# Kernel optimization log

Measured on AMD Instinct MI355X. Metric: run time of the kernel, lower is better.

## Reference

```python
import jax, jax.numpy as jnp
import numpy as np

KNOW = 128
EXER_N = 20000
STU_N = 50000
N_EDGES = 1000000
N_EDGES_P = 950000
BATCH = 8192
SOFT_PARA = 0.2
EPS = 1e-8


def setup_inputs() -> dict:
    key = jax.random.key(0)
    ks = jax.random.split(key, 10)
    return {
        'stu_emb': jax.random.normal(ks[0], (STU_N, KNOW), jnp.float32) * 0.1,
        'exer_emb': jax.random.normal(ks[1], (EXER_N, KNOW), jnp.float32) * 0.1,
        'W_ue': jax.random.normal(ks[2], (KNOW, KNOW), jnp.float32) / np.sqrt(KNOW),
        'W_ue_per': jax.random.normal(ks[3], (KNOW, KNOW), jnp.float32) / np.sqrt(KNOW),
        'W_deep': jax.random.normal(ks[4], (KNOW, KNOW), jnp.float32) / np.sqrt(KNOW),
        'src_e': jax.random.randint(ks[5], (N_EDGES,), 0, EXER_N),
        'dst_e': jax.random.randint(ks[6], (N_EDGES,), 0, STU_N),
        'src_p': jax.random.randint(ks[7], (N_EDGES_P,), 0, EXER_N),
        'dst_p': jax.random.randint(ks[8], (N_EDGES_P,), 0, STU_N),
        'stu_id': jax.random.randint(ks[9], (BATCH,), 0, STU_N),
    }


def _graph_layer(exer, W, src, dst):
    # u_from_e: messages flow exercise -> student. Linear transform then mean-aggregate.
    msg = exer[src] @ W                                   # [E_edges, K]
    agg = jax.ops.segment_sum(msg, dst, num_segments=STU_N)
    deg = jax.ops.segment_sum(jnp.ones_like(dst, jnp.float32), dst, num_segments=STU_N)
    return agg / jnp.maximum(deg, 1.0)[:, None]           # [STU_N, K]


def reference(stu_emb, exer_emb, W_ue, W_ue_per, W_deep, src_e, dst_e, src_p, dst_p, stu_id):
    # ExpressionDooubleEva: two parallel graph views
    stu1 = stu_emb + _graph_layer(exer_emb, W_ue, src_e, dst_e)
    stu_per = stu_emb + _graph_layer(exer_emb, W_ue_per, src_p, dst_p)
    # ExpressionSingleEva (u_from_e output is overwritten by u_from_e_deep in source)
    stu2 = stu1 + _graph_layer(exer_emb, W_deep, src_e, dst_e)
    stu2_per = stu_per + _graph_layer(exer_emb, W_deep, src_e, dst_e)

    b1 = stu2[stu_id]          # [B, K]
    b2 = stu2_per[stu_id]      # [B, K]
    n1 = b1 / jnp.linalg.norm(b1, axis=1, keepdims=True)
    n2 = b2 / jnp.linalg.norm(b2, axis=1, keepdims=True)
    sim = (n1 @ n2.T) / SOFT_PARA                         # [B, B]
    # faithful to source: numerator = exp(diag(sim)), denominator = sum of RAW sim row
    diag_exp = jnp.exp(jnp.diagonal(sim))
    row_sum = jnp.sum(sim, axis=1)
    ratio = diag_exp / (row_sum + EPS)
    ssl_loss = jnp.mean(-jnp.log(jnp.maximum(ratio, EPS)))
    return stu2, ssl_loss
```

## Files before the change

### kernel.cpp

```cpp
#include <hip/hip_runtime.h>
#include <math.h>

#define KNOW 128
#define STU_N 50000
#define EXER_N 20000
#define BATCH 8192
#define NE 1000000
#define NEP 950000
#define SOFT_INV 5.0f
#define EPS 1e-8f

#define CAP 64
#define NBIN 256
#define SPB 196
#define SSE 4608
#define SSP 1536
#define P1B 256
#define P1T 1024
#define WPB 24

typedef unsigned short u16;
typedef unsigned int u32;

typedef __attribute__((ext_vector_type(8))) short bf16x8;
typedef __attribute__((ext_vector_type(4))) float f32x4;

__device__ __forceinline__ u16 f2bf(float f) {
  union { float f; u32 u; } v;
  v.f = f;
  u32 r = (v.u + 0x7FFFu + ((v.u >> 16) & 1u)) >> 16;
  return (u16)r;
}
__device__ __forceinline__ float bflo(u32 u) {
  union { u32 u; float f; } v;
  v.u = u << 16;
  return v.f;
}
__device__ __forceinline__ float bfhi(u32 u) {
  union { u32 u; float f; } v;
  v.u = u & 0xFFFF0000u;
  return v.f;
}
__device__ __forceinline__ float bfu(u16 h) {
  union { u32 u; float f; } v;
  v.u = ((u32)h) << 16;
  return v.f;
}

__global__ void set_flags(const int* __restrict__ stu_id,
                          unsigned char* __restrict__ flag,
                          int* __restrict__ gcur_e, int* __restrict__ gcur_p) {
  int i = blockIdx.x * blockDim.x + threadIdx.x;
  if (i < BATCH) flag[stu_id[i]] = 1;
  if (i < NBIN) {
    gcur_e[i] = i * SSE;
    gcur_p[i] = i * SSP;
  }
}

__global__ __launch_bounds__(256) void prep_split(
    const float* __restrict__ exer, const float* __restrict__ W_ue,
    const float* __restrict__ W_per, const float* __restrict__ W_deep,
    u16* __restrict__ Ah, u16* __restrict__ Al, u16* __restrict__ WTh,
    u16* __restrict__ WTl) {
  int b = blockIdx.x;
  if (b < WPB) {
    int plane = b >> 3;
    int slab = b & 7;
    int t = threadIdx.x;
    int n = t & 127;
    int k0 = slab * 16 + (t >> 7) * 8;
    const float* W0 = (plane == 0) ? W_ue : (plane == 1) ? W_per : W_deep;
    float x[8];
#pragma unroll
    for (int j = 0; j < 8; ++j) {
      float v = W0[(k0 + j) * KNOW + n];
      if (plane == 0) v += W_deep[(k0 + j) * KNOW + n];
      x[j] = v;
    }
    u16 hi[8], lo[8];
#pragma unroll
    for (int j = 0; j < 8; ++j) {
      u16 h = f2bf(x[j]);
      hi[j] = h;
      lo[j] = f2bf(x[j] - bfu(h));
    }
    size_t base = ((size_t)plane * KNOW + n) * KNOW + k0;
    uint4 H = {(u32)hi[0] | ((u32)hi[1] << 16), (u32)hi[2] | ((u32)hi[3] << 16),
               (u32)hi[4] | ((u32)hi[5] << 16), (u32)hi[6] | ((u32)hi[7] << 16)};
    uint4 L = {(u32)lo[0] | ((u32)lo[1] << 16), (u32)lo[2] | ((u32)lo[3] << 16),
               (u32)lo[4] | ((u32)lo[5] << 16), (u32)lo[6] | ((u32)lo[7] << 16)};
    *(uint4*)(WTh + base) = H;
    *(uint4*)(WTl + base) = L;
  } else {
    size_t i = ((size_t)(b - WPB) * 256 + threadIdx.x) * 4;
    float4 v = *(const float4*)(exer + i);
    u16 h0 = f2bf(v.x), h1 = f2bf(v.y), h2 = f2bf(v.z), h3 = f2bf(v.w);
    ushort4 H = {h0, h1, h2, h3};
    ushort4 L = {f2bf(v.x - bfu(h0)), f2bf(v.y - bfu(h1)), f2bf(v.z - bfu(h2)),
                 f2bf(v.w - bfu(h3))};
    *(ushort4*)(Ah + i) = H;
    *(ushort4*)(Al + i) = L;
  }
}

#define BM_T 80

__global__ __launch_bounds__(512) void transform_mfma(
    const u16* __restrict__ Ah, const u16* __restrict__ Al,
    const u16* __restrict__ WTh, const u16* __restrict__ WTl,
    u16* __restrict__ X_sum, u16* __restrict__ X_per,
    u16* __restrict__ X_deep) {
  int t = threadIdx.x;
  int wv = t >> 6;
  int l = t & 63;
  int bn = l & 15;
  int kb = l >> 4;
  int row0 = blockIdx.x * BM_T;
  int n = wv * 16 + bn;

#pragma unroll 1
  for (int which = 0; which < 3; ++which) {
    u16* outp = (which == 0) ? X_sum : (which == 1) ? X_per : X_deep;
    const u16* wth = WTh + (size_t)which * KNOW * KNOW;
    const u16* wtl = WTl + (size_t)which * KNOW * KNOW;
    bf16x8 bh[4], bl[4];
#pragma unroll
    for (int ks = 0; ks < 4; ++ks) {
      int off = n * KNOW + ks * 32 + kb * 8;
      bh[ks] = *(const bf16x8*)(wth + off);
      bl[ks] = *(const bf16x8*)(wtl + off);
    }
#pragma unroll 1
    for (int rt = 0; rt < 5; ++rt) {
      int row = row0 + rt * 16 + bn;
      const u16* ap = Ah + (size_t)row * KNOW + kb * 8;
      const u16* alp = Al + (size_t)row * KNOW + kb * 8;
      f32x4 acc = {0.f, 0.f, 0.f, 0.f};
#pragma unroll
      for (int ks = 0; ks < 4; ++ks) {
        bf16x8 af = *(const bf16x8*)(ap + ks * 32);
        bf16x8 lf = *(const bf16x8*)(alp + ks * 32);
        acc = __builtin_amdgcn_mfma_f32_16x16x32_bf16(af, bh[ks], acc, 0, 0, 0);
        acc = __builtin_amdgcn_mfma_f32_16x16x32_bf16(lf, bh[ks], acc, 0, 0, 0);
        acc = __builtin_amdgcn_mfma_f32_16x16x32_bf16(af, bl[ks], acc, 0, 0, 0);
      }
      int orow = row0 + rt * 16 + kb * 4;
#pragma unroll
      for (int r = 0; r < 4; ++r)
        outp[(size_t)(orow + r) * KNOW + n] = f2bf(acc[r]);
    }
  }
}

__global__ __launch_bounds__(P1T) void bin_pass1(
    const int* __restrict__ dst_e, const int* __restrict__ src_e,
    const int* __restrict__ dst_p, const int* __restrict__ src_p,
    const unsigned char* __restrict__ flag, int* __restrict__ gcur_e,
    int* __restrict__ gcur_p, u32* __restrict__ stag_e,
    u32* __restrict__ stag_p) {
  __shared__ int cntE[NBIN], cntP[NBIN];
  __shared__ int baseE[NBIN], baseP[NBIN];
  __shared__ int curE[NBIN], curP[NBIN];
  int t = threadIdx.x;
  if (t < NBIN) {
    cntE[t] = 0;
    cntP[t] = 0;
  }
  __syncthreads();
  int b = blockIdx.x;
  int e0 = (int)((long long)NE * b / P1B);
  int e1 = (int)((long long)NE * (b + 1) / P1B);
  int p0 = (int)((long long)NEP * b / P1B);
  int p1 = (int)((long long)NEP * (b + 1) / P1B);
  for (int i = e0 + t; i < e1; i += P1T) {
    int d = __builtin_nontemporal_load(&dst_e[i]);
    atomicAdd(&cntE[d / SPB], 1);
  }
  for (int i = p0 + t; i < p1; i += P1T) {
    int d = __builtin_nontemporal_load(&dst_p[i]);
    if (flag[d]) atomicAdd(&cntP[d / SPB], 1);
  }
  __syncthreads();
  if (t < NBIN) {
    baseE[t] = atomicAdd(&gcur_e[t], cntE[t]);
    baseP[t] = atomicAdd(&gcur_p[t], cntP[t]);
    curE[t] = 0;
    curP[t] = 0;
  }
  __syncthreads();
  for (int i = e0 + t; i < e1; i += P1T) {
    int d = __builtin_nontemporal_load(&dst_e[i]);
    int s = __builtin_nontemporal_load(&src_e[i]);
    int bin = d / SPB;
    int pos = baseE[bin] + atomicAdd(&curE[bin], 1);
    if (pos < (bin + 1) * SSE)
      stag_e[pos] = ((u32)(d - bin * SPB) << 16) | (u32)s;
  }
  for (int i = p0 + t; i < p1; i += P1T) {
    int d = __builtin_nontemporal_load(&dst_p[i]);
    if (!flag[d]) continue;
    int s = __builtin_nontemporal_load(&src_p[i]);
    int bin = d / SPB;
    int pos = baseP[bin] + atomicAdd(&curP[bin], 1);
    if (pos < (bin + 1) * SSP)
      stag_p[pos] = ((u32)(d - bin * SPB) << 16) | (u32)s;
  }
}

__global__ __launch_bounds__(256) void bin_pass2(
    const u32* __restrict__ stag_e, const u32* __restrict__ stag_p,
    const int* __restrict__ gcur_e, const int* __restrict__ gcur_p,
    u16* __restrict__ bucket_e, u16* __restrict__ bucket_p,
    int* __restrict__ cnt_e, int* __restrict__ cnt_p) {
  __shared__ u16 be[SPB * CAP];
  __shared__ u16 bp[SPB * CAP];
  __shared__ int ce[SPB], cp[SPB];
  int t = threadIdx.x;
  int bin = blockIdx.x;
  for (int i = t; i < SPB; i += 256) {
    ce[i] = 0;
    cp[i] = 0;
  }
  __syncthreads();
  int ne = gcur_e[bin] - bin * SSE;
  if (ne > SSE) ne = SSE;
  int np = gcur_p[bin] - bin * SSP;
  if (np > SSP) np = SSP;
  const u32* se = stag_e + (size_t)bin * SSE;
  for (int i = t; i < ne; i += 256) {
    u32 w = se[i];
    int dl = (int)(w >> 16), s = (int)(w & 0xFFFFu);
    int slot = atomicAdd(&ce[dl], 1);
    if (slot < CAP) be[dl * CAP + slot] = (u16)s;
  }
  const u32* sp = stag_p + (size_t)bin * SSP;
  for (int i = t; i < np; i += 256) {
    u32 w = sp[i];
    int dl = (int)(w >> 16), s = (int)(w & 0xFFFFu);
    int slot = atomicAdd(&cp[dl], 1);
    if (slot < CAP) bp[dl * CAP + slot] = (u16)s;
  }
  __syncthreads();
  int s0 = bin * SPB;
  int nstu = STU_N - s0;
  if (nstu > SPB) nstu = SPB;
  if (nstu <= 0) return;
  int nvec = nstu * CAP * 2 / 16;
  const uint4* bev = (const uint4*)be;
  uint4* ge = (uint4*)(bucket_e + (size_t)s0 * CAP);
  for (int i = t; i < nvec; i += 256) ge[i] = bev[i];
  const uint4* bpv = (const uint4*)bp;
  uint4* gp = (uint4*)(bucket_p + (size_t)s0 * CAP);
  for (int i = t; i < nvec; i += 256) gp[i] = bpv[i];
  for (int i = t; i < nstu; i += 256) {
    cnt_e[s0 + i] = ce[i];
    cnt_p[s0 + i] = cp[i];
  }
}

__global__ __launch_bounds__(256) void stu2_gather(
    const float* __restrict__ stu_emb, const u16* __restrict__ X_sum,
    const u16* __restrict__ bucket, const int* __restrict__ cnt,
    float* __restrict__ out) {
  int wv = threadIdx.x >> 6;
  int l = threadIdx.x & 63;
  int s = blockIdx.x * 4 + wv;
  if (s >= STU_N) return;
  int deg = cnt[s];
  int e = (deg < CAP) ? deg : CAP;
  const u16* brow = bucket + (size_t)s * CAP;
  u32 bval = brow[l];
  int g = l >> 4;
  int c = l & 15;
  float acc[8] = {};
  for (int i = g; i < e; i += 8) {
    int r1 = __shfl((int)bval, i);
    const uint4 q1 = *(const uint4*)(X_sum + (size_t)r1 * KNOW + c * 8);
    int i2 = i + 4;
    int j2 = (i2 < e) ? i2 : (e - 1);
    int r2 = __shfl((int)bval, j2);
    const uint4 q2 = *(const uint4*)(X_sum + (size_t)r2 * KNOW + c * 8);
    float w2 = (i2 < e) ? 1.0f : 0.0f;
    acc[0] += bflo(q1.x) + w2 * bflo(q2.x);
    acc[1] += bfhi(q1.x) + w2 * bfhi(q2.x);
    acc[2] += bflo(q1.y) + w2 * bflo(q2.y);
    acc[3] += bfhi(q1.y) + w2 * bfhi(q2.y);
    acc[4] += bflo(q1.z) + w2 * bflo(q2.z);
    acc[5] += bfhi(q1.z) + w2 * bfhi(q2.z);
    acc[6] += bflo(q1.w) + w2 * bflo(q2.w);
    acc[7] += bfhi(q1.w) + w2 * bfhi(q2.w);
  }
#pragma unroll
  for (int j = 0; j < 8; ++j) {
    float v = acc[j];
    v += __shfl_xor(v, 16);
    v += __shfl_xor(v, 32);
    acc[j] = v;
  }
  if (l < 16) {
    float inv = 1.0f / fmaxf((float)deg, 1.0f);
    float4 se0 = *(const float4*)(stu_emb + (size_t)s * KNOW + c * 8);
    float4 se1 = *(const float4*)(stu_emb + (size_t)s * KNOW + c * 8 + 4);
    float4 o0 = {se0.x + acc[0] * inv, se0.y + acc[1] * inv,
                 se0.z + acc[2] * inv, se0.w + acc[3] * inv};
    float4 o1 = {se1.x + acc[4] * inv, se1.y + acc[5] * inv,
                 se1.z + acc[6] * inv, se1.w + acc[7] * inv};
    *(float4*)(out + (size_t)s * KNOW + c * 8) = o0;
    *(float4*)(out + (size_t)s * KNOW + c * 8 + 4) = o1;
  }
}

__global__ __launch_bounds__(128) void batch_kernel(
    const float* __restrict__ stu_emb, const float* __restrict__ stu2,
    const u16* __restrict__ X_per, const u16* __restrict__ X_deep,
    const u16* __restrict__ bucket_p, const int* __restrict__ cnt_p,
    const u16* __restrict__ bucket_e, const int* __restrict__ cnt_e,
    const int* __restrict__ stu_id, float* __restrict__ n1,
    float* __restrict__ n2, float* __restrict__ diag) {
  __shared__ float red[128];
  int i = blockIdx.x;
  int k = threadIdx.x;
  int sid = stu_id[i];

  int degp = cnt_p[sid];
  int ep = (degp < CAP) ? degp : CAP;
  const u16* brp = bucket_p + (size_t)sid * CAP;
  float accp = 0.0f;
  int j = 0;
  for (; j + 4 <= ep; j += 4) {
    int s0 = brp[j], s1 = brp[j + 1], s2 = brp[j + 2], s3 = brp[j + 3];
    accp += bfu(X_per[(size_t)s0 * KNOW + k]);
    accp += bfu(X_per[(size_t)s1 * KNOW + k]);
    accp += bfu(X_per[(size_t)s2 * KNOW + k]);
    accp += bfu(X_per[(size_t)s3 * KNOW + k]);
  }
  for (; j < ep; ++j) accp += bfu(X_per[(size_t)brp[j] * KNOW + k]);
  accp /= fmaxf((float)degp, 1.0f);

  int degd = cnt_e[sid];
  int ed = (degd < CAP) ? degd : CAP;
  const u16* brd = bucket_e + (size_t)sid * CAP;
  float accd = 0.0f;
  j = 0;
  for (; j + 4 <= ed; j += 4) {
    int s0 = brd[j], s1 = brd[j + 1], s2 = brd[j + 2], s3 = brd[j + 3];
    accd += bfu(X_deep[(size_t)s0 * KNOW + k]);
    accd += bfu(X_deep[(size_t)s1 * KNOW + k]);
    accd += bfu(X_deep[(size_t)s2 * KNOW + k]);
    accd += bfu(X_deep[(size_t)s3 * KNOW + k]);
  }
  for (; j < ed; ++j) accd += bfu(X_deep[(size_t)brd[j] * KNOW + k]);
  accd /= fmaxf((float)degd, 1.0f);

  float b1 = stu2[(size_t)sid * KNOW + k];
  float b2 = stu_emb[(size_t)sid * KNOW + k] + accp + accd;

  red[k] = b1 * b1;
  __syncthreads();
  for (int s = 64; s > 0; s >>= 1) {
    if (k < s) red[k] += red[k + s];
    __syncthreads();
  }
  float norm1 = sqrtf(red[0]);
  __syncthreads();
  red[k] = b2 * b2;
  __syncthreads();
  for (int s = 64; s > 0; s >>= 1) {
    if (k < s) red[k] += red[k + s];
    __syncthreads();
  }
  float norm2 = sqrtf(red[0]);

  float v1 = b1 / norm1;
  float v2 = b2 / norm2;
  n1[(size_t)i * KNOW + k] = v1;
  n2[(size_t)i * KNOW + k] = v2;

  __syncthreads();
  red[k] = v1 * v2;
  __syncthreads();
  for (int s = 64; s > 0; s >>= 1) {
    if (k < s) red[k] += red[k + s];
    __syncthreads();
  }
  if (k == 0) diag[i] = red[0];
}

__global__ __launch_bounds__(128) void s2_reduce(const float* __restrict__ n2,
                                                 float* __restrict__ S2) {
  int k = threadIdx.x;
  int r0 = blockIdx.x * (BATCH / 64);
  float acc = 0.0f;
  for (int r = 0; r < BATCH / 64; ++r) acc += n2[(size_t)(r0 + r) * KNOW + k];
  atomicAdd(&S2[k], acc);
}

#define L2BLKS 64
__global__ __launch_bounds__(256) void loss2(const float* __restrict__ n1,
                                             const float* __restrict__ diag,
                                             const float* __restrict__ S2,
                                             float* __restrict__ loss) {
  __shared__ float s2s[KNOW];
  int t = threadIdx.x;
  if (t < KNOW) s2s[t] = S2[t];
  __syncthreads();
  int wave = t >> 6, lane = t & 63;
  const int rows_per_wave = BATCH / (L2BLKS * 4);
  int r0 = (blockIdx.x * 4 + wave) * rows_per_wave;
  float acc = 0.0f;
  for (int r = r0; r < r0 + rows_per_wave; ++r) {
    float v = n1[(size_t)r * KNOW + lane] * s2s[lane] +
              n1[(size_t)r * KNOW + 64 + lane] * s2s[64 + lane];
#pragma unroll
    for (int off = 32; off > 0; off >>= 1) v += __shfl_down(v, off);
    if (lane == 0) {
      float rs = v * SOFT_INV;
      float dg = diag[r] * SOFT_INV;
      float ratio = expf(dg) / (rs + EPS);
      acc += -logf(fmaxf(ratio, EPS));
    }
  }
  if (lane == 0) atomicAdd(loss, acc);
}

__global__ void finalize_kernel(const float* __restrict__ loss,
                                float* __restrict__ out) {
  out[(size_t)STU_N * KNOW] = loss[0] * (1.0f / (float)BATCH);
}

extern "C" void kernel_launch(void* const* d_in, const int* in_sizes, int n_in,
                              void* d_out, int out_size, void* d_ws,
                              size_t ws_size, hipStream_t stream) {
  const float* stu_emb = (const float*)d_in[0];
  const float* exer_emb = (const float*)d_in[1];
  const float* W_ue = (const float*)d_in[2];
  const float* W_ue_per = (const float*)d_in[3];
  const float* W_deep = (const float*)d_in[4];
  const int* src_e = (const int*)d_in[5];
  const int* dst_e = (const int*)d_in[6];
  const int* src_p = (const int*)d_in[7];
  const int* dst_p = (const int*)d_in[8];
  const int* stu_id = (const int*)d_in[9];
  float* out = (float*)d_out;

  char* wsb = (char*)d_ws;
  float* S2 = (float*)wsb;
  float* loss = S2 + KNOW;
  unsigned char* flag = (unsigned char*)(loss + 1);
  size_t zero_bytes = (size_t)(flag + ((STU_N + 3) & ~3) - (unsigned char*)wsb);
  int* cnt_e = (int*)(flag + ((STU_N + 3) & ~3));
  int* cnt_p = cnt_e + STU_N;
  int* gcur_e = cnt_p + STU_N;
  int* gcur_p = gcur_e + NBIN;
  u16* X_sum = (u16*)(gcur_p + NBIN);
  u16* X_per = X_sum + (size_t)EXER_N * KNOW;
  u16* X_deep = X_per + (size_t)EXER_N * KNOW;
  u16* bucket_e = X_deep + (size_t)EXER_N * KNOW;
  u16* bucket_p = bucket_e + (size_t)STU_N * CAP;
  u32* stag_e = (u32*)(bucket_p + (size_t)STU_N * CAP);
  u32* stag_p = stag_e + (size_t)NBIN * SSE;
  float* n1 = (float*)(stag_p + (size_t)NBIN * SSP);
  float* n2 = n1 + (size_t)BATCH * KNOW;
  float* diag = n2 + (size_t)BATCH * KNOW;

  u16* Ah = (u16*)stag_e;
  u16* Al = (u16*)n1;
  u16* WTh = Al + (size_t)EXER_N * KNOW;
  u16* WTl = WTh + (size_t)3 * KNOW * KNOW;

  hipMemsetAsync(d_ws, 0, zero_bytes, stream);

  set_flags<<<(BATCH + 255) / 256, 256, 0, stream>>>(stu_id, flag, gcur_e,
                                                     gcur_p);

  prep_split<<<WPB + EXER_N * KNOW / 1024, 256, 0, stream>>>(
      exer_emb, W_ue, W_ue_per, W_deep, Ah, Al, WTh, WTl);

  transform_mfma<<<EXER_N / BM_T, 512, 0, stream>>>(Ah, Al, WTh, WTl, X_sum,
                                                    X_per, X_deep);

  bin_pass1<<<P1B, P1T, 0, stream>>>(dst_e, src_e, dst_p, src_p, flag, gcur_e,
                                     gcur_p, stag_e, stag_p);

  bin_pass2<<<NBIN, 256, 0, stream>>>(stag_e, stag_p, gcur_e, gcur_p, bucket_e,
                                      bucket_p, cnt_e, cnt_p);

  stu2_gather<<<(STU_N + 3) / 4, 256, 0, stream>>>(stu_emb, X_sum, bucket_e,
                                                   cnt_e, out);

  batch_kernel<<<BATCH, 128, 0, stream>>>(stu_emb, out, X_per, X_deep,
                                          bucket_p, cnt_p, bucket_e, cnt_e,
                                          stu_id, n1, n2, diag);

  s2_reduce<<<64, 128, 0, stream>>>(n2, S2);

  loss2<<<L2BLKS, 256, 0, stream>>>(n1, diag, S2, loss);

  finalize_kernel<<<1, 1, 0, stream>>>(loss, out);
}
```

Before: 280.9 us.

## Replace two-pass binned bucketing with single-pass global-atomic bucket build

Removes the two-kernel binning scheme (per-block shared-memory histograms, staging buffer, then per-bin LDS bucket assembly) and builds the per-student CSR-like buckets in one kernel using global atomicAdd on per-student counters with direct scattered u16 writes. This drops a kernel launch and the staging round-trip but adds about 1M contended global atomics and uncoalesced 2-byte scattered stores. The gather loop also replaces the multiply-by-mask with a branch for the second row, and the workspace is re-laid out so the split buffers no longer alias the staging area.

```diff
diff --git a/kernel.cpp b/kernel.cpp
--- a/kernel.cpp
+++ b/kernel.cpp
@@ -11,12 +11,7 @@
 #define EPS 1e-8f
 
 #define CAP 64
-#define NBIN 256
-#define SPB 196
-#define SSE 4608
-#define SSP 1536
-#define P1B 256
-#define P1T 1024
+#define BBB 1024
 #define WPB 24
 
 typedef unsigned short u16;
@@ -48,13 +43,31 @@
 }
 
 __global__ void set_flags(const int* __restrict__ stu_id,
-                          unsigned char* __restrict__ flag,
-                          int* __restrict__ gcur_e, int* __restrict__ gcur_p) {
+                          unsigned char* __restrict__ flag) {
   int i = blockIdx.x * blockDim.x + threadIdx.x;
   if (i < BATCH) flag[stu_id[i]] = 1;
-  if (i < NBIN) {
-    gcur_e[i] = i * SSE;
-    gcur_p[i] = i * SSP;
+}
+
+__global__ __launch_bounds__(256) void build_buckets(
+    const int* __restrict__ dst_e, const int* __restrict__ src_e,
+    const int* __restrict__ dst_p, const int* __restrict__ src_p,
+    const unsigned char* __restrict__ flag, int* __restrict__ cnt_e,
+    int* __restrict__ cnt_p, u16* __restrict__ bucket_e,
+    u16* __restrict__ bucket_p) {
+  int tid = blockIdx.x * 256 + threadIdx.x;
+  const int stride = BBB * 256;
+  for (int i = tid; i < NE; i += stride) {
+    int d = __builtin_nontemporal_load(&dst_e[i]);
+    int s = __builtin_nontemporal_load(&src_e[i]);
+    int slot = atomicAdd(&cnt_e[d], 1);
+    if (slot < CAP) bucket_e[(size_t)d * CAP + slot] = (u16)s;
+  }
+  for (int i = tid; i < NEP; i += stride) {
+    int d = __builtin_nontemporal_load(&dst_p[i]);
+    if (!flag[d]) continue;
+    int s = __builtin_nontemporal_load(&src_p[i]);
+    int slot = atomicAdd(&cnt_p[d], 1);
+    if (slot < CAP) bucket_p[(size_t)d * CAP + slot] = (u16)s;
   }
 }
 
@@ -150,112 +163,6 @@
       for (int r = 0; r < 4; ++r)
         outp[(size_t)(orow + r) * KNOW + n] = f2bf(acc[r]);
     }
-  }
-}
-
-__global__ __launch_bounds__(P1T) void bin_pass1(
-    const int* __restrict__ dst_e, const int* __restrict__ src_e,
-    const int* __restrict__ dst_p, const int* __restrict__ src_p,
-    const unsigned char* __restrict__ flag, int* __restrict__ gcur_e,
-    int* __restrict__ gcur_p, u32* __restrict__ stag_e,
-    u32* __restrict__ stag_p) {
-  __shared__ int cntE[NBIN], cntP[NBIN];
-  __shared__ int baseE[NBIN], baseP[NBIN];
-  __shared__ int curE[NBIN], curP[NBIN];
-  int t = threadIdx.x;
-  if (t < NBIN) {
-    cntE[t] = 0;
-    cntP[t] = 0;
-  }
-  __syncthreads();
-  int b = blockIdx.x;
-  int e0 = (int)((long long)NE * b / P1B);
-  int e1 = (int)((long long)NE * (b + 1) / P1B);
-  int p0 = (int)((long long)NEP * b / P1B);
-  int p1 = (int)((long long)NEP * (b + 1) / P1B);
-  for (int i = e0 + t; i < e1; i += P1T) {
-    int d = __builtin_nontemporal_load(&dst_e[i]);
-    atomicAdd(&cntE[d / SPB], 1);
-  }
-  for (int i = p0 + t; i < p1; i += P1T) {
-    int d = __builtin_nontemporal_load(&dst_p[i]);
-    if (flag[d]) atomicAdd(&cntP[d / SPB], 1);
-  }
-  __syncthreads();
-  if (t < NBIN) {
-    baseE[t] = atomicAdd(&gcur_e[t], cntE[t]);
-    baseP[t] = atomicAdd(&gcur_p[t], cntP[t]);
-    curE[t] = 0;
-    curP[t] = 0;
-  }
-  __syncthreads();
-  for (int i = e0 + t; i < e1; i += P1T) {
-    int d = __builtin_nontemporal_load(&dst_e[i]);
-    int s = __builtin_nontemporal_load(&src_e[i]);
-    int bin = d / SPB;
-    int pos = baseE[bin] + atomicAdd(&curE[bin], 1);
-    if (pos < (bin + 1) * SSE)
-      stag_e[pos] = ((u32)(d - bin * SPB) << 16) | (u32)s;
-  }
-  for (int i = p0 + t; i < p1; i += P1T) {
-    int d = __builtin_nontemporal_load(&dst_p[i]);
-    if (!flag[d]) continue;
-    int s = __builtin_nontemporal_load(&src_p[i]);
-    int bin = d / SPB;
-    int pos = baseP[bin] + atomicAdd(&curP[bin], 1);
-    if (pos < (bin + 1) * SSP)
-      stag_p[pos] = ((u32)(d - bin * SPB) << 16) | (u32)s;
-  }
-}
-
-__global__ __launch_bounds__(256) void bin_pass2(
-    const u32* __restrict__ stag_e, const u32* __restrict__ stag_p,
-    const int* __restrict__ gcur_e, const int* __restrict__ gcur_p,
-    u16* __restrict__ bucket_e, u16* __restrict__ bucket_p,
-    int* __restrict__ cnt_e, int* __restrict__ cnt_p) {
-  __shared__ u16 be[SPB * CAP];
-  __shared__ u16 bp[SPB * CAP];
-  __shared__ int ce[SPB], cp[SPB];
-  int t = threadIdx.x;
-  int bin = blockIdx.x;
-  for (int i = t; i < SPB; i += 256) {
-    ce[i] = 0;
-    cp[i] = 0;
-  }
-  __syncthreads();
-  int ne = gcur_e[bin] - bin * SSE;
-  if (ne > SSE) ne = SSE;
-  int np = gcur_p[bin] - bin * SSP;
-  if (np > SSP) np = SSP;
-  const u32* se = stag_e + (size_t)bin * SSE;
-  for (int i = t; i < ne; i += 256) {
-    u32 w = se[i];
-    int dl = (int)(w >> 16), s = (int)(w & 0xFFFFu);
-    int slot = atomicAdd(&ce[dl], 1);
-    if (slot < CAP) be[dl * CAP + slot] = (u16)s;
-  }
-  const u32* sp = stag_p + (size_t)bin * SSP;
-  for (int i = t; i < np; i += 256) {
-    u32 w = sp[i];
-    int dl = (int)(w >> 16), s = (int)(w & 0xFFFFu);
-    int slot = atomicAdd(&cp[dl], 1);
-    if (slot < CAP) bp[dl * CAP + slot] = (u16)s;
-  }
-  __syncthreads();
-  int s0 = bin * SPB;
-  int nstu = STU_N - s0;
-  if (nstu > SPB) nstu = SPB;
-  if (nstu <= 0) return;
-  int nvec = nstu * CAP * 2 / 16;
-  const uint4* bev = (const uint4*)be;
-  uint4* ge = (uint4*)(bucket_e + (size_t)s0 * CAP);
-  for (int i = t; i < nvec; i += 256) ge[i] = bev[i];
-  const uint4* bpv = (const uint4*)bp;
-  uint4* gp = (uint4*)(bucket_p + (size_t)s0 * CAP);
-  for (int i = t; i < nvec; i += 256) gp[i] = bpv[i];
-  for (int i = t; i < nstu; i += 256) {
-    cnt_e[s0 + i] = ce[i];
-    cnt_p[s0 + i] = cp[i];
   }
 }
 
@@ -278,18 +185,27 @@
     int r1 = __shfl((int)bval, i);
     const uint4 q1 = *(const uint4*)(X_sum + (size_t)r1 * KNOW + c * 8);
     int i2 = i + 4;
-    int j2 = (i2 < e) ? i2 : (e - 1);
+    int j2 = (i2 < e) ? i2 : i;
     int r2 = __shfl((int)bval, j2);
     const uint4 q2 = *(const uint4*)(X_sum + (size_t)r2 * KNOW + c * 8);
-    float w2 = (i2 < e) ? 1.0f : 0.0f;
-    acc[0] += bflo(q1.x) + w2 * bflo(q2.x);
-    acc[1] += bfhi(q1.x) + w2 * bfhi(q2.x);
-    acc[2] += bflo(q1.y) + w2 * bflo(q2.y);
-    acc[3] += bfhi(q1.y) + w2 * bfhi(q2.y);
-    acc[4] += bflo(q1.z) + w2 * bflo(q2.z);
-    acc[5] += bfhi(q1.z) + w2 * bfhi(q2.z);
-    acc[6] += bflo(q1.w) + w2 * bflo(q2.w);
-    acc[7] += bfhi(q1.w) + w2 * bfhi(q2.w);
+    acc[0] += bflo(q1.x);
+    acc[1] += bfhi(q1.x);
+    acc[2] += bflo(q1.y);
+    acc[3] += bfhi(q1.y);
+    acc[4] += bflo(q1.z);
+    acc[5] += bfhi(q1.z);
+    acc[6] += bflo(q1.w);
+    acc[7] += bfhi(q1.w);
+    if (i2 < e) {
+      acc[0] += bflo(q2.x);
+      acc[1] += bfhi(q2.x);
+      acc[2] += bflo(q2.y);
+      acc[3] += bfhi(q2.y);
+      acc[4] += bflo(q2.z);
+      acc[5] += bfhi(q2.z);
+      acc[6] += bflo(q2.w);
+      acc[7] += bfhi(q2.w);
+    }
   }
 #pragma unroll
   for (int j = 0; j < 8; ++j) {
@@ -448,31 +364,26 @@
   float* S2 = (float*)wsb;
   float* loss = S2 + KNOW;
   unsigned char* flag = (unsigned char*)(loss + 1);
-  size_t zero_bytes = (size_t)(flag + ((STU_N + 3) & ~3) - (unsigned char*)wsb);
   int* cnt_e = (int*)(flag + ((STU_N + 3) & ~3));
   int* cnt_p = cnt_e + STU_N;
-  int* gcur_e = cnt_p + STU_N;
-  int* gcur_p = gcur_e + NBIN;
-  u16* X_sum = (u16*)(gcur_p + NBIN);
+  size_t zero_bytes = (size_t)((char*)(cnt_p + STU_N) - wsb);
+  char* rest = wsb + ((zero_bytes + 63) & ~(size_t)63);
+  u16* X_sum = (u16*)rest;
   u16* X_per = X_sum + (size_t)EXER_N * KNOW;
   u16* X_deep = X_per + (size_t)EXER_N * KNOW;
   u16* bucket_e = X_deep + (size_t)EXER_N * KNOW;
   u16* bucket_p = bucket_e + (size_t)STU_N * CAP;
-  u32* stag_e = (u32*)(bucket_p + (size_t)STU_N * CAP);
-  u32* stag_p = stag_e + (size_t)NBIN * SSE;
-  float* n1 = (float*)(stag_p + (size_t)NBIN * SSP);
+  float* n1 = (float*)(bucket_p + (size_t)STU_N * CAP);
   float* n2 = n1 + (size_t)BATCH * KNOW;
   float* diag = n2 + (size_t)BATCH * KNOW;
-
-  u16* Ah = (u16*)stag_e;
-  u16* Al = (u16*)n1;
+  u16* Ah = (u16*)(diag + BATCH);
+  u16* Al = Ah + (size_t)EXER_N * KNOW;
   u16* WTh = Al + (size_t)EXER_N * KNOW;
   u16* WTl = WTh + (size_t)3 * KNOW * KNOW;
 
   hipMemsetAsync(d_ws, 0, zero_bytes, stream);
 
-  set_flags<<<(BATCH + 255) / 256, 256, 0, stream>>>(stu_id, flag, gcur_e,
-                                                     gcur_p);
+  set_flags<<<(BATCH + 255) / 256, 256, 0, stream>>>(stu_id, flag);
 
   prep_split<<<WPB + EXER_N * KNOW / 1024, 256, 0, stream>>>(
       exer_emb, W_ue, W_ue_per, W_deep, Ah, Al, WTh, WTl);
@@ -480,11 +391,8 @@
   transform_mfma<<<EXER_N / BM_T, 512, 0, stream>>>(Ah, Al, WTh, WTl, X_sum,
                                                     X_per, X_deep);
 
-  bin_pass1<<<P1B, P1T, 0, stream>>>(dst_e, src_e, dst_p, src_p, flag, gcur_e,
-                                     gcur_p, stag_e, stag_p);
-
-  bin_pass2<<<NBIN, 256, 0, stream>>>(stag_e, stag_p, gcur_e, gcur_p, bucket_e,
-                                      bucket_p, cnt_e, cnt_p);
+  build_buckets<<<BBB, 256, 0, stream>>>(dst_e, src_e, dst_p, src_p, flag,
+                                         cnt_e, cnt_p, bucket_e, bucket_p);
 
   stu2_gather<<<(STU_N + 3) / 4, 256, 0, stream>>>(stu_emb, X_sum, bucket_e,
                                                    cnt_e, out);
```

Result: slower. 334.0 us (+18.9%).

## Rewrite batch kernel as wave-per-row vectorized gather with shuffle reductions

Applied to the files above, without the earlier changes.

The batch kernel now gives each batch row to one 64-lane wavefront instead of a 128-thread block. Each lane gathers bf16 rows with 16-byte loads, driven by shuffled bucket indices, and the block-wide shared-memory tree reductions with their many barriers are replaced by xor-shuffle reductions. The student-row gather now skips the unused second load with a branch instead of multiplying by a zero weight. Workspace buffers are laid out separately, so the split A matrices no longer alias the staging and n1 buffers, which uses more workspace memory.

```diff
diff --git a/kernel.cpp b/kernel.cpp
--- a/kernel.cpp
+++ b/kernel.cpp
@@ -55,6 +55,112 @@
   if (i < NBIN) {
     gcur_e[i] = i * SSE;
     gcur_p[i] = i * SSP;
+  }
+}
+
+__global__ __launch_bounds__(P1T) void bin_pass1(
+    const int* __restrict__ dst_e, const int* __restrict__ src_e,
+    const int* __restrict__ dst_p, const int* __restrict__ src_p,
+    const unsigned char* __restrict__ flag, int* __restrict__ gcur_e,
+    int* __restrict__ gcur_p, u32* __restrict__ stag_e,
+    u32* __restrict__ stag_p) {
+  __shared__ int cntE[NBIN], cntP[NBIN];
+  __shared__ int baseE[NBIN], baseP[NBIN];
+  __shared__ int curE[NBIN], curP[NBIN];
+  int t = threadIdx.x;
+  if (t < NBIN) {
+    cntE[t] = 0;
+    cntP[t] = 0;
+  }
+  __syncthreads();
+  int b = blockIdx.x;
+  int e0 = (int)((long long)NE * b / P1B);
+  int e1 = (int)((long long)NE * (b + 1) / P1B);
+  int p0 = (int)((long long)NEP * b / P1B);
+  int p1 = (int)((long long)NEP * (b + 1) / P1B);
+  for (int i = e0 + t; i < e1; i += P1T) {
+    int d = __builtin_nontemporal_load(&dst_e[i]);
+    atomicAdd(&cntE[d / SPB], 1);
+  }
+  for (int i = p0 + t; i < p1; i += P1T) {
+    int d = __builtin_nontemporal_load(&dst_p[i]);
+    if (flag[d]) atomicAdd(&cntP[d / SPB], 1);
+  }
+  __syncthreads();
+  if (t < NBIN) {
+    baseE[t] = atomicAdd(&gcur_e[t], cntE[t]);
+    baseP[t] = atomicAdd(&gcur_p[t], cntP[t]);
+    curE[t] = 0;
+    curP[t] = 0;
+  }
+  __syncthreads();
+  for (int i = e0 + t; i < e1; i += P1T) {
+    int d = __builtin_nontemporal_load(&dst_e[i]);
+    int s = __builtin_nontemporal_load(&src_e[i]);
+    int bin = d / SPB;
+    int pos = baseE[bin] + atomicAdd(&curE[bin], 1);
+    if (pos < (bin + 1) * SSE)
+      stag_e[pos] = ((u32)(d - bin * SPB) << 16) | (u32)s;
+  }
+  for (int i = p0 + t; i < p1; i += P1T) {
+    int d = __builtin_nontemporal_load(&dst_p[i]);
+    if (!flag[d]) continue;
+    int s = __builtin_nontemporal_load(&src_p[i]);
+    int bin = d / SPB;
+    int pos = baseP[bin] + atomicAdd(&curP[bin], 1);
+    if (pos < (bin + 1) * SSP)
+      stag_p[pos] = ((u32)(d - bin * SPB) << 16) | (u32)s;
+  }
+}
+
+__global__ __launch_bounds__(256) void bin_pass2(
+    const u32* __restrict__ stag_e, const u32* __restrict__ stag_p,
+    const int* __restrict__ gcur_e, const int* __restrict__ gcur_p,
+    u16* __restrict__ bucket_e, u16* __restrict__ bucket_p,
+    int* __restrict__ cnt_e, int* __restrict__ cnt_p) {
+  __shared__ u16 be[SPB * CAP];
+  __shared__ u16 bp[SPB * CAP];
+  __shared__ int ce[SPB], cp[SPB];
+  int t = threadIdx.x;
+  int bin = blockIdx.x;
+  for (int i = t; i < SPB; i += 256) {
+    ce[i] = 0;
+    cp[i] = 0;
+  }
+  __syncthreads();
+  int ne = gcur_e[bin] - bin * SSE;
+  if (ne > SSE) ne = SSE;
+  int np = gcur_p[bin] - bin * SSP;
+  if (np > SSP) np = SSP;
+  const u32* se = stag_e + (size_t)bin * SSE;
+  for (int i = t; i < ne; i += 256) {
+    u32 w = se[i];
+    int dl = (int)(w >> 16), s = (int)(w & 0xFFFFu);
+    int slot = atomicAdd(&ce[dl], 1);
+    if (slot < CAP) be[dl * CAP + slot] = (u16)s;
+  }
+  const u32* sp = stag_p + (size_t)bin * SSP;
+  for (int i = t; i < np; i += 256) {
+    u32 w = sp[i];
+    int dl = (int)(w >> 16), s = (int)(w & 0xFFFFu);
+    int slot = atomicAdd(&cp[dl], 1);
+    if (slot < CAP) bp[dl * CAP + slot] = (u16)s;
+  }
+  __syncthreads();
+  int s0 = bin * SPB;
+  int nstu = STU_N - s0;
+  if (nstu > SPB) nstu = SPB;
+  if (nstu <= 0) return;
+  int nvec = nstu * CAP * 2 / 16;
+  const uint4* bev = (const uint4*)be;
+  uint4* ge = (uint4*)(bucket_e + (size_t)s0 * CAP);
+  for (int i = t; i < nvec; i += 256) ge[i] = bev[i];
+  const uint4* bpv = (const uint4*)bp;
+  uint4* gp = (uint4*)(bucket_p + (size_t)s0 * CAP);
+  for (int i = t; i < nvec; i += 256) gp[i] = bpv[i];
+  for (int i = t; i < nstu; i += 256) {
+    cnt_e[s0 + i] = ce[i];
+    cnt_p[s0 + i] = cp[i];
   }
 }
 
@@ -150,112 +256,6 @@
       for (int r = 0; r < 4; ++r)
         outp[(size_t)(orow + r) * KNOW + n] = f2bf(acc[r]);
     }
-  }
-}
-
-__global__ __launch_bounds__(P1T) void bin_pass1(
-    const int* __restrict__ dst_e, const int* __restrict__ src_e,
-    const int* __restrict__ dst_p, const int* __restrict__ src_p,
-    const unsigned char* __restrict__ flag, int* __restrict__ gcur_e,
-    int* __restrict__ gcur_p, u32* __restrict__ stag_e,
-    u32* __restrict__ stag_p) {
-  __shared__ int cntE[NBIN], cntP[NBIN];
-  __shared__ int baseE[NBIN], baseP[NBIN];
-  __shared__ int curE[NBIN], curP[NBIN];
-  int t = threadIdx.x;
-  if (t < NBIN) {
-    cntE[t] = 0;
-    cntP[t] = 0;
-  }
-  __syncthreads();
-  int b = blockIdx.x;
-  int e0 = (int)((long long)NE * b / P1B);
-  int e1 = (int)((long long)NE * (b + 1) / P1B);
-  int p0 = (int)((long long)NEP * b / P1B);
-  int p1 = (int)((long long)NEP * (b + 1) / P1B);
-  for (int i = e0 + t; i < e1; i += P1T) {
-    int d = __builtin_nontemporal_load(&dst_e[i]);
-    atomicAdd(&cntE[d / SPB], 1);
-  }
-  for (int i = p0 + t; i < p1; i += P1T) {
-    int d = __builtin_nontemporal_load(&dst_p[i]);
-    if (flag[d]) atomicAdd(&cntP[d / SPB], 1);
-  }
-  __syncthreads();
-  if (t < NBIN) {
-    baseE[t] = atomicAdd(&gcur_e[t], cntE[t]);
-    baseP[t] = atomicAdd(&gcur_p[t], cntP[t]);
-    curE[t] = 0;
-    curP[t] = 0;
-  }
-  __syncthreads();
-  for (int i = e0 + t; i < e1; i += P1T) {
-    int d = __builtin_nontemporal_load(&dst_e[i]);
-    int s = __builtin_nontemporal_load(&src_e[i]);
-    int bin = d / SPB;
-    int pos = baseE[bin] + atomicAdd(&curE[bin], 1);
-    if (pos < (bin + 1) * SSE)
-      stag_e[pos] = ((u32)(d - bin * SPB) << 16) | (u32)s;
-  }
-  for (int i = p0 + t; i < p1; i += P1T) {
-    int d = __builtin_nontemporal_load(&dst_p[i]);
-    if (!flag[d]) continue;
-    int s = __builtin_nontemporal_load(&src_p[i]);
-    int bin = d / SPB;
-    int pos = baseP[bin] + atomicAdd(&curP[bin], 1);
-    if (pos < (bin + 1) * SSP)
-      stag_p[pos] = ((u32)(d - bin * SPB) << 16) | (u32)s;
-  }
-}
-
-__global__ __launch_bounds__(256) void bin_pass2(
-    const u32* __restrict__ stag_e, const u32* __restrict__ stag_p,
-    const int* __restrict__ gcur_e, const int* __restrict__ gcur_p,
-    u16* __restrict__ bucket_e, u16* __restrict__ bucket_p,
-    int* __restrict__ cnt_e, int* __restrict__ cnt_p) {
-  __shared__ u16 be[SPB * CAP];
-  __shared__ u16 bp[SPB * CAP];
-  __shared__ int ce[SPB], cp[SPB];
-  int t = threadIdx.x;
-  int bin = blockIdx.x;
-  for (int i = t; i < SPB; i += 256) {
-    ce[i] = 0;
-    cp[i] = 0;
-  }
-  __syncthreads();
-  int ne = gcur_e[bin] - bin * SSE;
-  if (ne > SSE) ne = SSE;
-  int np = gcur_p[bin] - bin * SSP;
-  if (np > SSP) np = SSP;
-  const u32* se = stag_e + (size_t)bin * SSE;
-  for (int i = t; i < ne; i += 256) {
-    u32 w = se[i];
-    int dl = (int)(w >> 16), s = (int)(w & 0xFFFFu);
-    int slot = atomicAdd(&ce[dl], 1);
-    if (slot < CAP) be[dl * CAP + slot] = (u16)s;
-  }
-  const u32* sp = stag_p + (size_t)bin * SSP;
-  for (int i = t; i < np; i += 256) {
-    u32 w = sp[i];
-    int dl = (int)(w >> 16), s = (int)(w & 0xFFFFu);
-    int slot = atomicAdd(&cp[dl], 1);
-    if (slot < CAP) bp[dl * CAP + slot] = (u16)s;
-  }
-  __syncthreads();
-  int s0 = bin * SPB;
-  int nstu = STU_N - s0;
-  if (nstu > SPB) nstu = SPB;
-  if (nstu <= 0) return;
-  int nvec = nstu * CAP * 2 / 16;
-  const uint4* bev = (const uint4*)be;
-  uint4* ge = (uint4*)(bucket_e + (size_t)s0 * CAP);
-  for (int i = t; i < nvec; i += 256) ge[i] = bev[i];
-  const uint4* bpv = (const uint4*)bp;
-  uint4* gp = (uint4*)(bucket_p + (size_t)s0 * CAP);
-  for (int i = t; i < nvec; i += 256) gp[i] = bpv[i];
-  for (int i = t; i < nstu; i += 256) {
-    cnt_e[s0 + i] = ce[i];
-    cnt_p[s0 + i] = cp[i];
   }
 }
 
@@ -278,18 +278,27 @@
     int r1 = __shfl((int)bval, i);
     const uint4 q1 = *(const uint4*)(X_sum + (size_t)r1 * KNOW + c * 8);
     int i2 = i + 4;
-    int j2 = (i2 < e) ? i2 : (e - 1);
+    int j2 = (i2 < e) ? i2 : i;
     int r2 = __shfl((int)bval, j2);
     const uint4 q2 = *(const uint4*)(X_sum + (size_t)r2 * KNOW + c * 8);
-    float w2 = (i2 < e) ? 1.0f : 0.0f;
-    acc[0] += bflo(q1.x) + w2 * bflo(q2.x);
-    acc[1] += bfhi(q1.x) + w2 * bfhi(q2.x);
-    acc[2] += bflo(q1.y) + w2 * bflo(q2.y);
-    acc[3] += bfhi(q1.y) + w2 * bfhi(q2.y);
-    acc[4] += bflo(q1.z) + w2 * bflo(q2.z);
-    acc[5] += bfhi(q1.z) + w2 * bfhi(q2.z);
-    acc[6] += bflo(q1.w) + w2 * bflo(q2.w);
-    acc[7] += bfhi(q1.w) + w2 * bfhi(q2.w);
+    acc[0] += bflo(q1.x);
+    acc[1] += bfhi(q1.x);
+    acc[2] += bflo(q1.y);
+    acc[3] += bfhi(q1.y);
+    acc[4] += bflo(q1.z);
+    acc[5] += bfhi(q1.z);
+    acc[6] += bflo(q1.w);
+    acc[7] += bfhi(q1.w);
+    if (i2 < e) {
+      acc[0] += bflo(q2.x);
+      acc[1] += bfhi(q2.x);
+      acc[2] += bflo(q2.y);
+      acc[3] += bfhi(q2.y);
+      acc[4] += bflo(q2.z);
+      acc[5] += bfhi(q2.z);
+      acc[6] += bflo(q2.w);
+      acc[7] += bfhi(q2.w);
+    }
   }
 #pragma unroll
   for (int j = 0; j < 8; ++j) {
@@ -311,80 +320,120 @@
   }
 }
 
-__global__ __launch_bounds__(128) void batch_kernel(
+__global__ __launch_bounds__(256) void batch_kernel(
     const float* __restrict__ stu_emb, const float* __restrict__ stu2,
     const u16* __restrict__ X_per, const u16* __restrict__ X_deep,
     const u16* __restrict__ bucket_p, const int* __restrict__ cnt_p,
     const u16* __restrict__ bucket_e, const int* __restrict__ cnt_e,
     const int* __restrict__ stu_id, float* __restrict__ n1,
     float* __restrict__ n2, float* __restrict__ diag) {
-  __shared__ float red[128];
-  int i = blockIdx.x;
-  int k = threadIdx.x;
+  int wv = threadIdx.x >> 6;
+  int l = threadIdx.x & 63;
+  int i = blockIdx.x * 4 + wv;
   int sid = stu_id[i];
+  int g = l >> 4;
+  int c = l & 15;
 
   int degp = cnt_p[sid];
   int ep = (degp < CAP) ? degp : CAP;
-  const u16* brp = bucket_p + (size_t)sid * CAP;
-  float accp = 0.0f;
-  int j = 0;
-  for (; j + 4 <= ep; j += 4) {
-    int s0 = brp[j], s1 = brp[j + 1], s2 = brp[j + 2], s3 = brp[j + 3];
-    accp += bfu(X_per[(size_t)s0 * KNOW + k]);
-    accp += bfu(X_per[(size_t)s1 * KNOW + k]);
-    accp += bfu(X_per[(size_t)s2 * KNOW + k]);
-    accp += bfu(X_per[(size_t)s3 * KNOW + k]);
-  }
-  for (; j < ep; ++j) accp += bfu(X_per[(size_t)brp[j] * KNOW + k]);
-  accp /= fmaxf((float)degp, 1.0f);
+  u32 bvp = bucket_p[(size_t)sid * CAP + l];
+  float ap[8] = {};
+  for (int t = g; t < ep; t += 8) {
+    int r1 = __shfl((int)bvp, t);
+    const uint4 q1 = *(const uint4*)(X_per + (size_t)r1 * KNOW + c * 8);
+    int t2 = t + 4;
+    int j2 = (t2 < ep) ? t2 : t;
+    int r2 = __shfl((int)bvp, j2);
+    const uint4 q2 = *(const uint4*)(X_per + (size_t)r2 * KNOW + c * 8);
+    ap[0] += bflo(q1.x); ap[1] += bfhi(q1.x);
+    ap[2] += bflo(q1.y); ap[3] += bfhi(q1.y);
+    ap[4] += bflo(q1.z); ap[5] += bfhi(q1.z);
+    ap[6] += bflo(q1.w); ap[7] += bfhi(q1.w);
+    if (t2 < ep) {
+      ap[0] += bflo(q2.x); ap[1] += bfhi(q2.x);
+      ap[2] += bflo(q2.y); ap[3] += bfhi(q2.y);
+      ap[4] += bflo(q2.z); ap[5] += bfhi(q2.z);
+      ap[6] += bflo(q2.w); ap[7] += bfhi(q2.w);
+    }
+  }
 
   int degd = cnt_e[sid];
   int ed = (degd < CAP) ? degd : CAP;
-  const u16* brd = bucket_e + (size_t)sid * CAP;
-  float accd = 0.0f;
-  j = 0;
-  for (; j + 4 <= ed; j += 4) {
-    int s0 = brd[j], s1 = brd[j + 1], s2 = brd[j + 2], s3 = brd[j + 3];
-    accd += bfu(X_deep[(size_t)s0 * KNOW + k]);
-    accd += bfu(X_deep[(size_t)s1 * KNOW + k]);
-    accd += bfu(X_deep[(size_t)s2 * KNOW + k]);
-    accd += bfu(X_deep[(size_t)s3 * KNOW + k]);
-  }
-  for (; j < ed; ++j) accd += bfu(X_deep[(size_t)brd[j] * KNOW + k]);
-  accd /= fmaxf((float)degd, 1.0f);
-
-  float b1 = stu2[(size_t)sid * KNOW + k];
-  float b2 = stu_emb[(size_t)sid * KNOW + k] + accp + accd;
-
-  red[k] = b1 * b1;
-  __syncthreads();
-  for (int s = 64; s > 0; s >>= 1) {
-    if (k < s) red[k] += red[k + s];
-    __syncthreads();
-  }
-  float norm1 = sqrtf(red[0]);
-  __syncthreads();
-  red[k] = b2 * b2;
-  __syncthreads();
-  for (int s = 64; s > 0; s >>= 1) {
-    if (k < s) red[k] += red[k + s];
-    __syncthreads();
-  }
-  float norm2 = sqrtf(red[0]);
-
-  float v1 = b1 / norm1;
-  float v2 = b2 / norm2;
-  n1[(size_t)i * KNOW + k] = v1;
-  n2[(size_t)i * KNOW + k] = v2;
-
-  __syncthreads();
-  red[k] = v1 * v2;
-  __syncthreads();
-  for (int s = 64; s > 0; s >>= 1) {
-    if (k < s) red[k] += red[k + s];
-    __syncthreads();
-  }
-  if (k == 0) diag[i] = red[0];
+  u32 bvd = bucket_e[(size_t)sid * CAP + l];
+  float ad[8] = {};
+  for (int t = g; t < ed; t += 8) {
+    int r1 = __shfl((int)bvd, t);
+    const uint4 q1 = *(const uint4*)(X_deep + (size_t)r1 * KNOW + c * 8);
+    int t2 = t + 4;
+    int j2 = (t2 < ed) ? t2 : t;
+    int r2 = __shfl((int)bvd, j2);
+    const uint4 q2 = *(const uint4*)(X_deep + (size_t)r2 * KNOW + c * 8);
+    ad[0] += bflo(q1.x); ad[1] += bfhi(q1.x);
+    ad[2] += bflo(q1.y); ad[3] += bfhi(q1.y);
+    ad[4] += bflo(q1.z); ad[5] += bfhi(q1.z);
+    ad[6] += bflo(q1.w); ad[7] += bfhi(q1.w);
+    if (t2 < ed) {
+      ad[0] += bflo(q2.x); ad[1] += bfhi(q2.x);
+      ad[2] += bflo(q2.y); ad[3] += bfhi(q2.y);
+      ad[4] += bflo(q2.z); ad[5] += bfhi(q2.z);
+      ad[6] += bflo(q2.w); ad[7] += bfhi(q2.w);
+    }
+  }
+
+#pragma unroll
+  for (int j = 0; j < 8; ++j) {
+    float v = ap[j];
+    v += __shfl_xor(v, 16);
+    v += __shfl_xor(v, 32);
+    ap[j] = v;
+    float w = ad[j];
+    w += __shfl_xor(w, 16);
+    w += __shfl_xor(w, 32);
+    ad[j] = w;
+  }
+
+  float invp = 1.0f / fmaxf((float)degp, 1.0f);
+  float invd = 1.0f / fmaxf((float)degd, 1.0f);
+  float4 e0 = *(const float4*)(stu_emb + (size_t)sid * KNOW + c * 8);
+  float4 e1 = *(const float4*)(stu_emb + (size_t)sid * KNOW + c * 8 + 4);
+  float4 s0 = *(const float4*)(stu2 + (size_t)sid * KNOW + c * 8);
+  float4 s1 = *(const float4*)(stu2 + (size_t)sid * KNOW + c * 8 + 4);
+  float b1v[8] = {s0.x, s0.y, s0.z, s0.w, s1.x, s1.y, s1.z, s1.w};
+  float ev[8] = {e0.x, e0.y, e0.z, e0.w, e1.x, e1.y, e1.z, e1.w};
+  float b2v[8];
+  float s11 = 0.f, s22 = 0.f, s12 = 0.f;
+#pragma unroll
+  for (int j = 0; j < 8; ++j) {
+    b2v[j] = ev[j] + ap[j] * invp + ad[j] * invd;
+    s11 += b1v[j] * b1v[j];
+    s22 += b2v[j] * b2v[j];
+    s12 += b1v[j] * b2v[j];
+  }
+#pragma unroll
+  for (int off = 1; off <= 8; off <<= 1) {
+    s11 += __shfl_xor(s11, off);
+    s22 += __shfl_xor(s22, off);
+    s12 += __shfl_xor(s12, off);
+  }
+  float norm1 = sqrtf(s11);
+  float norm2 = sqrtf(s22);
+  if (g == 0) {
+    float4 o0 = {b1v[0] / norm1, b1v[1] / norm1, b1v[2] / norm1,
+                 b1v[3] / norm1};
+    float4 o1 = {b1v[4] / norm1, b1v[5] / norm1, b1v[6] / norm1,
+                 b1v[7] / norm1};
+    *(float4*)(n1 + (size_t)i * KNOW + c * 8) = o0;
+    *(float4*)(n1 + (size_t)i * KNOW + c * 8 + 4) = o1;
+  } else if (g == 1) {
+    float4 o0 = {b2v[0] / norm2, b2v[1] / norm2, b2v[2] / norm2,
+                 b2v[3] / norm2};
+    float4 o1 = {b2v[4] / norm2, b2v[5] / norm2, b2v[6] / norm2,
+                 b2v[7] / norm2};
+    *(float4*)(n2 + (size_t)i * KNOW + c * 8) = o0;
+    *(float4*)(n2 + (size_t)i * KNOW + c * 8 + 4) = o1;
+  } else if (g == 2 && c == 0) {
+    diag[i] = s12 / (norm1 * norm2);
+  }
 }
 
 __global__ __launch_bounds__(128) void s2_reduce(const float* __restrict__ n2,
@@ -448,8 +497,9 @@
   float* S2 = (float*)wsb;
   float* loss = S2 + KNOW;
   unsigned char* flag = (unsigned char*)(loss + 1);
-  size_t zero_bytes = (size_t)(flag + ((STU_N + 3) & ~3) - (unsigned char*)wsb);
-  int* cnt_e = (int*)(flag + ((STU_N + 3) & ~3));
+  size_t zero_bytes = (size_t)((char*)flag + STU_N - wsb);
+  char* rest = wsb + ((zero_bytes + 63) & ~(size_t)63);
+  int* cnt_e = (int*)rest;
   int* cnt_p = cnt_e + STU_N;
   int* gcur_e = cnt_p + STU_N;
   int* gcur_p = gcur_e + NBIN;
@@ -463,9 +513,8 @@
   float* n1 = (float*)(stag_p + (size_t)NBIN * SSP);
   float* n2 = n1 + (size_t)BATCH * KNOW;
   float* diag = n2 + (size_t)BATCH * KNOW;
-
-  u16* Ah = (u16*)stag_e;
-  u16* Al = (u16*)n1;
+  u16* Ah = (u16*)(diag + BATCH);
+  u16* Al = Ah + (size_t)EXER_N * KNOW;
   u16* WTh = Al + (size_t)EXER_N * KNOW;
   u16* WTl = WTh + (size_t)3 * KNOW * KNOW;
 
@@ -489,9 +538,9 @@
   stu2_gather<<<(STU_N + 3) / 4, 256, 0, stream>>>(stu_emb, X_sum, bucket_e,
                                                    cnt_e, out);
 
-  batch_kernel<<<BATCH, 128, 0, stream>>>(stu_emb, out, X_per, X_deep,
-                                          bucket_p, cnt_p, bucket_e, cnt_e,
-                                          stu_id, n1, n2, diag);
+  batch_kernel<<<BATCH / 4, 256, 0, stream>>>(stu_emb, out, X_per, X_deep,
+                                              bucket_p, cnt_p, bucket_e, cnt_e,
+                                              stu_id, n1, n2, diag);
 
   s2_reduce<<<64, 128, 0, stream>>>(n2, S2);
 
```

Measured after the change: 269.6 us. -4.0%, faster.
